# Kernel optimization log

Measured on AMD Instinct MI355X. Metric: run time of the kernel, lower is better.

## Reference

```python
import jax, jax.numpy as jnp
import numpy as np

IN_F = 4096
OUT_F = 4096
Q_RANK = 2
R_RANK = 2
SCALE = 1.0
B, S = 2, 2048


def setup_inputs() -> dict:
    key = jax.random.key(0)
    ks = jax.random.split(key, 8)
    inp = jax.random.normal(ks[0], (B, S, IN_F), jnp.float32)
    # Q, R come from a QR decomposition of linear.weight.t(); random stand-ins with
    # matching shapes and O(1) scale are fine for a numerical baseline.
    Q = jax.random.normal(ks[1], (IN_F, OUT_F), jnp.float32) / np.sqrt(IN_F).astype(np.float32)
    R = jax.random.normal(ks[2], (OUT_F, OUT_F), jnp.float32) / np.sqrt(OUT_F).astype(np.float32)
    # kron_Q1/Q2 are initialized to identity in __init__ (never re-initialized);
    # add small noise so the rotation path is non-trivial.
    sq1 = IN_F // Q_RANK
    kron_Q1 = jnp.eye(sq1, dtype=jnp.float32) + 0.01 * jax.random.normal(ks[3], (sq1, sq1), jnp.float32)
    kron_Q2 = jnp.eye(Q_RANK, dtype=jnp.float32) + 0.01 * jax.random.normal(ks[4], (Q_RANK, Q_RANK), jnp.float32)
    # kron_R1/R2 use normal init with std = 1/size.
    sr1 = OUT_F // R_RANK
    kron_R1 = jax.random.normal(ks[5], (sr1, sr1), jnp.float32) / sr1
    kron_R2 = jax.random.normal(ks[6], (R_RANK, R_RANK), jnp.float32) / R_RANK
    # lambda_matrix inits to zeros; use small noise so the delta term is exercised.
    lambda_matrix = 0.01 * jax.random.normal(ks[7], (OUT_F,), jnp.float32)
    return {"input": inp, "Q": Q, "R": R, "kron_Q1": kron_Q1, "kron_Q2": kron_Q2,
            "kron_R1": kron_R1, "kron_R2": kron_R2, "lambda_matrix": lambda_matrix}


def reference(input, Q, R, kron_Q1, kron_Q2, kron_R1, kron_R2, lambda_matrix):
    rotation = jnp.kron(kron_Q1, kron_Q2)          # [in, in]
    orth = jnp.kron(kron_R1, kron_R2)              # [out, out]
    # orth @ diag(lambda) @ orth.T without materializing diag
    R_eff = R + (orth * lambda_matrix[None, :]) @ orth.T  # [out, out]
    W_t = rotation @ (Q @ R_eff)                   # [in, out]
    # F.linear(input, W_t.t()) == input @ W_t; dropout is identity in eval; bias=False
    return (input @ W_t) * SCALE
```

## Files before the change

kernel.cpp:

```cpp
#include <hip/hip_runtime.h>
#include <stdint.h>


typedef unsigned short u16;
typedef short bf16x8 __attribute__((ext_vector_type(8)));
typedef float f32x4 __attribute__((ext_vector_type(4)));

__device__ __forceinline__ u16 f2bf(float f) {
  union { float f; uint32_t u; } v; v.f = f;
  return (u16)((v.u + 0x7FFFu + ((v.u >> 16) & 1u)) >> 16);
}

__device__ __forceinline__ void store_out(float* p, float v) { *p = v; }
__device__ __forceinline__ void store_out(u16* p, float v) { *p = f2bf(v); }

__device__ __forceinline__ void gload_lds16(const u16* g, u16* l) {
  __builtin_amdgcn_global_load_lds(
      (__attribute__((address_space(1))) void*)(uintptr_t)g,
      (__attribute__((address_space(3))) void*)l, 16, 0, 0);
}

#define MFMA16(a, b, c) __builtin_amdgcn_mfma_f32_16x16x32_bf16((a), (b), (c), 0, 0, 0)

template <typename OutT>
__global__ __launch_bounds__(512, 2) void gemm256(
    const u16* __restrict__ A, const u16* __restrict__ Bt, OutT* __restrict__ C,
    int M, int N, int K, int ldC, long long sA, long long sB, long long sC) {
  extern __shared__ __align__(16) u16 smem[];
  u16* ldsA = smem;
  u16* ldsB = smem + 32768;

  const int tid  = (int)threadIdx.x;
  const int lane = tid & 63;
  const int wid  = tid >> 6;
  const int wr   = wid >> 2;
  const int wc   = wid & 3;

  const int tilesX = (int)gridDim.x;
  const int tilesXY = tilesX * (int)gridDim.y;
  const int nwg = tilesXY * (int)gridDim.z;
  const int bid = ((int)blockIdx.z * (int)gridDim.y + (int)blockIdx.y) * tilesX + (int)blockIdx.x;
  const int swz = (bid & 7) * (nwg >> 3) + (bid >> 3);
  const int z   = swz / tilesXY;
  const int rem = swz % tilesXY;
  const int brow = (rem / tilesX) << 8;
  const int bcol = (rem % tilesX) << 8;
  A += (size_t)z * sA;
  Bt += (size_t)(z >> 1) * sB;
  C += (size_t)z * sC;

  const int lr = lane & 15, lg = lane >> 4, h = lr >> 1;
  const int sf = (lg + ((lr & 1) << 2)) ^ h;
  const int abase = wr * 8192 + h * 64 + sf * 8;
  const int bbase = (wc >> 1) * 8192 + ((wc & 1) * 32 + h) * 64 + sf * 8;

  const int kp   = (tid & 7) ^ ((tid >> 3) & 7);
  const int srow = 2 * (tid >> 3) + (kp >> 2);
  const int scol = (kp & 3) << 3;
  const size_t gA0 = (size_t)(brow + srow) * K + scol;
  const size_t gB0 = (size_t)(bcol + srow) * K + scol;
  const size_t rstep = (size_t)K << 7;
  const int sdst = wid * 512;

  const int NC = K >> 6;
  const int NI = NC >> 1;

  f32x4 acc[8][4] = {};
  bf16x8 af[4], bf[4][2];

#define STG_A(t, rh, ks) gload_lds16(A + gA0 + (rh) * rstep + (size_t)(t) * 64 + (ks) * 32, \
    ldsA + ((t) & 1) * 16384 + (rh) * 8192 + (ks) * 4096 + sdst)
#define STG_B(t, rh, ks) gload_lds16(Bt + gB0 + (rh) * rstep + (size_t)(t) * 64 + (ks) * 32, \
    ldsB + ((t) & 1) * 16384 + (rh) * 8192 + (ks) * 4096 + sdst)
#define VM4 asm volatile("s_waitcnt vmcnt(4)" ::: "memory")
#define VM0 asm volatile("s_waitcnt vmcnt(0)" ::: "memory")

#define PH(BUF, MH, KS, RDBF, S0, S1, TAIL) do {                                \
    const u16* _pa = ldsA + (BUF) * 16384 + abase + (KS) * 4096;                \
    const u16* _pb = ldsB + (BUF) * 16384 + bbase + (KS) * 4096;                \
    _Pragma("unroll")                                                           \
    for (int m = 0; m < 4; ++m)                                                 \
      af[m] = *(const bf16x8*)(_pa + ((MH) * 4 + m) * 512);                     \
    if (RDBF) {                                                                 \
      _Pragma("unroll")                                                         \
      for (int n = 0; n < 4; ++n)                                               \
        bf[n][KS] = *(const bf16x8*)(_pb + n * 512);                            \
    }                                                                           \
    S0; S1;                                                                     \
    __builtin_amdgcn_s_barrier();                                               \
    asm volatile("s_waitcnt lgkmcnt(0)" ::: "memory");                          \
    __builtin_amdgcn_sched_barrier(0);                                          \
    __builtin_amdgcn_s_setprio(1);                                              \
    _Pragma("unroll")                                                           \
    for (int m = 0; m < 4; ++m)                                                 \
      _Pragma("unroll")                                                         \
      for (int n = 0; n < 4; ++n)                                               \
        acc[(MH) * 4 + m][n] = MFMA16(af[m], bf[n][KS], acc[(MH) * 4 + m][n]);  \
    __builtin_amdgcn_s_setprio(0);                                              \
    TAIL;                                                                       \
    __builtin_amdgcn_sched_barrier(0);                                          \
    __builtin_amdgcn_s_barrier();                                               \
  } while (0)

  STG_A(0, 0, 0); STG_A(0, 0, 1); STG_A(0, 1, 0); STG_A(0, 1, 1);
  STG_B(0, 0, 0); STG_B(0, 0, 1); STG_B(0, 1, 0); STG_B(0, 1, 1);
  STG_B(1, 0, 0); STG_B(1, 0, 1); STG_B(1, 1, 0); STG_B(1, 1, 1);
  VM4;
  __builtin_amdgcn_sched_barrier(0);
  __builtin_amdgcn_s_barrier();

  for (int i = 0; i < NI - 1; ++i) {
    const int tn = 2 * i;
    PH(0, 0, 0, 1, STG_A(tn + 1, 0, 0), STG_A(tn + 1, 0, 1), (void)0);
    PH(0, 0, 1, 1, STG_A(tn + 1, 1, 0), STG_A(tn + 1, 1, 1), (void)0);
    PH(0, 1, 0, 0, STG_B(tn + 2, 0, 0), STG_B(tn + 2, 0, 1), (void)0);
    PH(0, 1, 1, 0, STG_B(tn + 2, 1, 0), STG_B(tn + 2, 1, 1), VM4);
    PH(1, 0, 0, 1, STG_A(tn + 2, 0, 0), STG_A(tn + 2, 0, 1), (void)0);
    PH(1, 0, 1, 1, STG_A(tn + 2, 1, 0), STG_A(tn + 2, 1, 1), (void)0);
    PH(1, 1, 0, 0, STG_B(tn + 3, 0, 0), STG_B(tn + 3, 0, 1), (void)0);
    PH(1, 1, 1, 0, STG_B(tn + 3, 1, 0), STG_B(tn + 3, 1, 1), VM4);
  }
  {
    PH(0, 0, 0, 1, STG_A(NC - 1, 0, 0), STG_A(NC - 1, 0, 1), (void)0);
    PH(0, 0, 1, 1, STG_A(NC - 1, 1, 0), STG_A(NC - 1, 1, 1), (void)0);
    PH(0, 1, 0, 0, (void)0, (void)0, (void)0);
    PH(0, 1, 1, 0, (void)0, (void)0, VM0);
    PH(1, 0, 0, 1, (void)0, (void)0, (void)0);
    PH(1, 0, 1, 1, (void)0, (void)0, (void)0);
    PH(1, 1, 0, 0, (void)0, (void)0, (void)0);
    PH(1, 1, 1, 0, (void)0, (void)0, (void)0);
  }

#undef PH
#undef STG_A
#undef STG_B
#undef VM4
#undef VM0

#pragma unroll
  for (int m = 0; m < 8; ++m) {
    const int r0 = brow + wr * 128 + m * 16 + lg * 4;
#pragma unroll
    for (int n = 0; n < 4; ++n) {
      const int cc = bcol + wc * 64 + n * 16 + lr;
#pragma unroll
      for (int j = 0; j < 4; ++j)
        store_out(&C[(size_t)(r0 + j) * ldC + cc], acc[m][n][j]);
    }
  }
}

__global__ void trans_kernel(const float* __restrict__ in, u16* __restrict__ out, int n) {
  __shared__ float t[32][33];
  const int bx = (int)blockIdx.x * 32, by = (int)blockIdx.y * 32;
  const int x = (int)threadIdx.x, y0 = (int)threadIdx.y;
#pragma unroll
  for (int dy = 0; dy < 32; dy += 8)
    t[y0 + dy][x] = in[(size_t)(bx + y0 + dy) * n + by + x];
  __syncthreads();
#pragma unroll
  for (int dy = 0; dy < 32; dy += 8)
    out[(size_t)(by + y0 + dy) * n + bx + x] = f2bf(t[x][y0 + dy]);
}

__global__ void transperm_kernel(const float* __restrict__ in, u16* __restrict__ out) {
  __shared__ float t[32][33];
  const int bx = (int)blockIdx.x * 32, by = (int)blockIdx.y * 32;
  const int x = (int)threadIdx.x, y0 = (int)threadIdx.y;
#pragma unroll
  for (int dy = 0; dy < 32; dy += 8)
    t[y0 + dy][x] = in[(size_t)(bx + y0 + dy) * 4096 + by + x];
  __syncthreads();
  const int r = bx + x;
  const int cp = ((r & 1) << 11) | (r >> 1);
#pragma unroll
  for (int dy = 0; dy < 32; dy += 8)
    out[(size_t)(by + y0 + dy) * 4096 + cp] = f2bf(t[x][y0 + dy]);
}

__global__ void transadd_kernel(const float* __restrict__ R, const float* __restrict__ Dsub,
                                const float* __restrict__ R2, u16* __restrict__ out) {
  __shared__ float t[32][33];
  const int bx = (int)blockIdx.x * 32, by = (int)blockIdx.y * 32;
  const int x = (int)threadIdx.x, y0 = (int)threadIdx.y;
#pragma unroll
  for (int dy = 0; dy < 32; dy += 8)
    t[y0 + dy][x] = R[(size_t)(bx + y0 + dy) * 4096 + by + x];
  __syncthreads();
  const float r20 = R2[0], r21 = R2[1], r22 = R2[2], r23 = R2[3];
  const int j = bx + x;
  const float cj0 = (j & 1) ? r22 : r20;
  const float cj1 = (j & 1) ? r23 : r21;
#pragma unroll
  for (int dy = 0; dy < 32; dy += 8) {
    const int i = by + y0 + dy;
    const float ci0 = (i & 1) ? r22 : r20;
    const float ci1 = (i & 1) ? r23 : r21;
    const size_t o = ((size_t)(i >> 1) << 11) + (j >> 1);
    const float de = Dsub[o] + Dsub[o + 2u * 4194304u];
    const float dd = Dsub[o + 4194304u] + Dsub[o + 3u * 4194304u];
    const float d = ci0 * cj0 * de + ci1 * cj1 * dd;
    out[(size_t)i * 4096 + j] = f2bf(t[x][y0 + dy] + d);
  }
}

__global__ void scale_r1_kernel(const float* __restrict__ R1, const float* __restrict__ lam,
                                u16* __restrict__ B2, u16* __restrict__ A4) {
  const int idx = (int)blockIdx.x * 256 + (int)threadIdx.x;
  const int i1 = idx >> 9, k1 = (idx & 511) << 2;
  const float4 r1 = *(const float4*)(R1 + (size_t)i1 * 2048 + k1);
  const float4 l0 = *(const float4*)(lam + 2 * k1);
  const float4 l1 = *(const float4*)(lam + 2 * k1 + 4);
  const int kh = k1 >> 10, kk = k1 & 1023;
  const size_t off = (size_t)i1 * 1024 + kk;
  const size_t P = 2097152;
  ushort4 rb, eb, ob;
  rb.x = f2bf(r1.x); rb.y = f2bf(r1.y); rb.z = f2bf(r1.z); rb.w = f2bf(r1.w);
  eb.x = f2bf(r1.x * l0.x); eb.y = f2bf(r1.y * l0.z);
  eb.z = f2bf(r1.z * l1.x); eb.w = f2bf(r1.w * l1.z);
  ob.x = f2bf(r1.x * l0.y); ob.y = f2bf(r1.y * l0.w);
  ob.z = f2bf(r1.z * l1.y); ob.w = f2bf(r1.w * l1.w);
  *(ushort4*)(B2 + (size_t)kh * P + off) = rb;
  *(ushort4*)(A4 + (size_t)(kh * 2) * P + off) = eb;
  *(ushort4*)(A4 + (size_t)(kh * 2 + 1) * P + off) = ob;
}

__global__ void tprep_kernel(const float* __restrict__ in, const float* __restrict__ Q2,
                             u16* __restrict__ T) {
  const int idx = (int)blockIdx.x * 256 + (int)threadIdx.x;
  const int s = idx >> 9, k1 = (idx & 511) << 2;
  const float4 a = *(const float4*)(in + (size_t)s * 4096 + 2 * k1);
  const float4 b = *(const float4*)(in + (size_t)s * 4096 + 2 * k1 + 4);
  const float e[4] = {a.x, a.z, b.x, b.z};
  const float o[4] = {a.y, a.w, b.y, b.w};
  const float q00 = Q2[0], q01 = Q2[1], q10 = Q2[2], q11 = Q2[3];
  ushort4 t0, t1;
  t0.x = f2bf(e[0] * q00 + o[0] * q10); t1.x = f2bf(e[0] * q01 + o[0] * q11);
  t0.y = f2bf(e[1] * q00 + o[1] * q10); t1.y = f2bf(e[1] * q01 + o[1] * q11);
  t0.z = f2bf(e[2] * q00 + o[2] * q10); t1.z = f2bf(e[2] * q01 + o[2] * q11);
  t0.w = f2bf(e[3] * q00 + o[3] * q10); t1.w = f2bf(e[3] * q01 + o[3] * q11);
  *(ushort4*)(T + (size_t)s * 2048 + k1) = t0;
  *(ushort4*)(T + 8388608 + (size_t)s * 2048 + k1) = t1;
}

extern "C" void kernel_launch(void* const* d_in, const int* in_sizes, int n_in,
                              void* d_out, int out_size, void* d_ws, size_t ws_size,
                              hipStream_t stream) {
  const float* input = (const float*)d_in[0];
  const float* Q     = (const float*)d_in[1];
  const float* R     = (const float*)d_in[2];
  const float* Q1    = (const float*)d_in[3];
  const float* Q2    = (const float*)d_in[4];
  const float* R1    = (const float*)d_in[5];
  const float* R2    = (const float*)d_in[6];
  const float* lam   = (const float*)d_in[7];
  float* out = (float*)d_out;

  const size_t MB = 1024ull * 1024ull;
  char* ws = (char*)d_ws;
  u16* B2    = (u16*)(ws + 0 * MB);
  u16* A4    = (u16*)(ws + 8 * MB);
  u16* Q1tb  = (u16*)(ws + 24 * MB);
  u16* T     = (u16*)(ws + 32 * MB);
  u16* Qtp   = (u16*)(ws + 64 * MB);
  u16* rteff = (u16*)(ws + 96 * MB);
  u16* X1p   = (u16*)(ws + 128 * MB);
  u16* X2    = (u16*)(ws + 8 * MB);
  float* Dsub = (float*)d_out;

  {
    void (*pf)(const u16*, const u16*, float*, int, int, int, int, long long, long long, long long) = gemm256<float>;
    void (*pb)(const u16*, const u16*, u16*, int, int, int, int, long long, long long, long long)   = gemm256<u16>;
    (void)hipFuncSetAttribute((const void*)pf, hipFuncAttributeMaxDynamicSharedMemorySize, 131072);
    (void)hipFuncSetAttribute((const void*)pb, hipFuncAttributeMaxDynamicSharedMemorySize, 131072);
  }

  const dim3 tb(32, 8);
  trans_kernel<<<dim3(64, 64), tb, 0, stream>>>(Q1, Q1tb, 2048);
  transperm_kernel<<<dim3(128, 128), tb, 0, stream>>>(Q, Qtp);
  scale_r1_kernel<<<4096, 256, 0, stream>>>(R1, lam, B2, A4);
  tprep_kernel<<<8192, 256, 0, stream>>>(input, Q2, T);
  gemm256<float><<<dim3(8, 8, 4), 512, 131072, stream>>>(
      A4, B2, Dsub, 2048, 2048, 1024, 2048, 2097152LL, 2097152LL, 4194304LL);
  transadd_kernel<<<dim3(128, 128), tb, 0, stream>>>(R, Dsub, R2, rteff);
  gemm256<u16><<<dim3(8, 16, 2), 512, 131072, stream>>>(
      T, Q1tb, X1p, 4096, 2048, 2048, 4096, 8388608LL, 0LL, 2048LL);
  gemm256<u16><<<dim3(16, 16, 1), 512, 131072, stream>>>(
      X1p, Qtp, X2, 4096, 4096, 4096, 4096, 0LL, 0LL, 0LL);
  gemm256<float><<<dim3(16, 16, 1), 512, 131072, stream>>>(
      X2, rteff, out, 4096, 4096, 4096, 4096, 0LL, 0LL, 0LL);
}
```

Measured before the change: 431.9 us.

## Shrink GEMM tile to 256x128 with triple-buffered BK=32 LDS pipeline

Reworks the bf16 MFMA GEMM from a 256x256 tile with double-buffered BK=64 stages to a 256x128 tile with a rotating three-buffer BK=32 pipeline. The 8 waves become a 4x2 grid, each computing 64x64, and all launch grids double in N. LDS drops to 72KB and launch bounds rise to 4 blocks per CU, aiming for more occupancy and better wave-level latency hiding. The costs are lower arithmetic intensity per tile, more global and L2 traffic for A, and a barrier pair every 32-wide k step.

Measured after the change: 510.5 us. 1.18x slower.

```diff
diff --git a/kernel.cpp b/kernel.cpp
--- a/kernel.cpp
+++ b/kernel.cpp
@@ -23,18 +23,18 @@
 #define MFMA16(a, b, c) __builtin_amdgcn_mfma_f32_16x16x32_bf16((a), (b), (c), 0, 0, 0)
 
 template <typename OutT>
-__global__ __launch_bounds__(512, 2) void gemm256(
+__global__ __launch_bounds__(512, 4) void gemm256(
     const u16* __restrict__ A, const u16* __restrict__ Bt, OutT* __restrict__ C,
     int M, int N, int K, int ldC, long long sA, long long sB, long long sC) {
   extern __shared__ __align__(16) u16 smem[];
   u16* ldsA = smem;
-  u16* ldsB = smem + 32768;
+  u16* ldsB = smem + 24576;
 
   const int tid  = (int)threadIdx.x;
   const int lane = tid & 63;
   const int wid  = tid >> 6;
-  const int wr   = wid >> 2;
-  const int wc   = wid & 3;
+  const int wr   = wid >> 1;
+  const int wc   = wid & 1;
 
   const int tilesX = (int)gridDim.x;
   const int tilesXY = tilesX * (int)gridDim.y;
@@ -44,15 +44,15 @@
   const int z   = swz / tilesXY;
   const int rem = swz % tilesXY;
   const int brow = (rem / tilesX) << 8;
-  const int bcol = (rem % tilesX) << 8;
+  const int bcol = (rem % tilesX) << 7;
   A += (size_t)z * sA;
   Bt += (size_t)(z >> 1) * sB;
   C += (size_t)z * sC;
 
   const int lr = lane & 15, lg = lane >> 4, h = lr >> 1;
   const int sf = (lg + ((lr & 1) << 2)) ^ h;
-  const int abase = wr * 8192 + h * 64 + sf * 8;
-  const int bbase = (wc >> 1) * 8192 + ((wc & 1) * 32 + h) * 64 + sf * 8;
+  const int abase = (wr >> 1) * 4096 + (wr & 1) * 2048 + h * 64 + sf * 8;
+  const int bbase = wc * 2048 + h * 64 + sf * 8;
 
   const int kp   = (tid & 7) ^ ((tid >> 3) & 7);
   const int srow = 2 * (tid >> 3) + (kp >> 2);
@@ -62,31 +62,35 @@
   const size_t rstep = (size_t)K << 7;
   const int sdst = wid * 512;
 
-  const int NC = K >> 6;
-  const int NI = NC >> 1;
-
-  f32x4 acc[8][4] = {};
-  bf16x8 af[4], bf[4][2];
-
-#define STG_A(t, rh, ks) gload_lds16(A + gA0 + (rh) * rstep + (size_t)(t) * 64 + (ks) * 32, \
-    ldsA + ((t) & 1) * 16384 + (rh) * 8192 + (ks) * 4096 + sdst)
-#define STG_B(t, rh, ks) gload_lds16(Bt + gB0 + (rh) * rstep + (size_t)(t) * 64 + (ks) * 32, \
-    ldsB + ((t) & 1) * 16384 + (rh) * 8192 + (ks) * 4096 + sdst)
-#define VM4 asm volatile("s_waitcnt vmcnt(4)" ::: "memory")
+  const int NC = K >> 5;
+
+  f32x4 acc[4][4] = {};
+  bf16x8 af[4], bf[4];
+
+  int aCur = 0, aNxt = 8192, aSpr = 16384;
+  int bCur = 0, bNxt = 4096, bSpr = 8192;
+
+#define STG_A(c, rh, dstOff) gload_lds16(A + gA0 + (rh) * rstep + (size_t)(c) * 32, \
+    ldsA + (dstOff) + (rh) * 4096 + sdst)
+#define STG_B(c, dstOff) gload_lds16(Bt + gB0 + (size_t)(c) * 32, ldsB + (dstOff) + sdst)
+#define STAGE(c, aOff, bOff) do { STG_A(c, 0, aOff); STG_A(c, 1, aOff); STG_B(c, bOff); } while (0)
+#define VM3 asm volatile("s_waitcnt vmcnt(3)" ::: "memory")
 #define VM0 asm volatile("s_waitcnt vmcnt(0)" ::: "memory")
 
-#define PH(BUF, MH, KS, RDBF, S0, S1, TAIL) do {                                \
-    const u16* _pa = ldsA + (BUF) * 16384 + abase + (KS) * 4096;                \
-    const u16* _pb = ldsB + (BUF) * 16384 + bbase + (KS) * 4096;                \
+  STAGE(0, 0, 0);
+  STAGE(1, 8192, 4096);
+  VM3;
+  __builtin_amdgcn_sched_barrier(0);
+  __builtin_amdgcn_s_barrier();
+
+#define PH(DOSTG, c2, TAIL) do {                                                \
+    const u16* _pa = ldsA + aCur + abase;                                       \
+    const u16* _pb = ldsB + bCur + bbase;                                       \
     _Pragma("unroll")                                                           \
-    for (int m = 0; m < 4; ++m)                                                 \
-      af[m] = *(const bf16x8*)(_pa + ((MH) * 4 + m) * 512);                     \
-    if (RDBF) {                                                                 \
-      _Pragma("unroll")                                                         \
-      for (int n = 0; n < 4; ++n)                                               \
-        bf[n][KS] = *(const bf16x8*)(_pb + n * 512);                            \
-    }                                                                           \
-    S0; S1;                                                                     \
+    for (int m = 0; m < 4; ++m) af[m] = *(const bf16x8*)(_pa + m * 512);        \
+    _Pragma("unroll")                                                           \
+    for (int n = 0; n < 4; ++n) bf[n] = *(const bf16x8*)(_pb + n * 512);        \
+    if (DOSTG) STAGE(c2, aSpr, bSpr);                                           \
     __builtin_amdgcn_s_barrier();                                               \
     asm volatile("s_waitcnt lgkmcnt(0)" ::: "memory");                          \
     __builtin_amdgcn_sched_barrier(0);                                          \
@@ -95,51 +99,29 @@
     for (int m = 0; m < 4; ++m)                                                 \
       _Pragma("unroll")                                                         \
       for (int n = 0; n < 4; ++n)                                               \
-        acc[(MH) * 4 + m][n] = MFMA16(af[m], bf[n][KS], acc[(MH) * 4 + m][n]);  \
+        acc[m][n] = MFMA16(af[m], bf[n], acc[m][n]);                            \
     __builtin_amdgcn_s_setprio(0);                                              \
     TAIL;                                                                       \
     __builtin_amdgcn_sched_barrier(0);                                          \
     __builtin_amdgcn_s_barrier();                                               \
+    const int _ta = aCur; aCur = aNxt; aNxt = aSpr; aSpr = _ta;                 \
+    const int _tb = bCur; bCur = bNxt; bNxt = bSpr; bSpr = _tb;                 \
   } while (0)
 
-  STG_A(0, 0, 0); STG_A(0, 0, 1); STG_A(0, 1, 0); STG_A(0, 1, 1);
-  STG_B(0, 0, 0); STG_B(0, 0, 1); STG_B(0, 1, 0); STG_B(0, 1, 1);
-  STG_B(1, 0, 0); STG_B(1, 0, 1); STG_B(1, 1, 0); STG_B(1, 1, 1);
-  VM4;
-  __builtin_amdgcn_sched_barrier(0);
-  __builtin_amdgcn_s_barrier();
-
-  for (int i = 0; i < NI - 1; ++i) {
-    const int tn = 2 * i;
-    PH(0, 0, 0, 1, STG_A(tn + 1, 0, 0), STG_A(tn + 1, 0, 1), (void)0);
-    PH(0, 0, 1, 1, STG_A(tn + 1, 1, 0), STG_A(tn + 1, 1, 1), (void)0);
-    PH(0, 1, 0, 0, STG_B(tn + 2, 0, 0), STG_B(tn + 2, 0, 1), (void)0);
-    PH(0, 1, 1, 0, STG_B(tn + 2, 1, 0), STG_B(tn + 2, 1, 1), VM4);
-    PH(1, 0, 0, 1, STG_A(tn + 2, 0, 0), STG_A(tn + 2, 0, 1), (void)0);
-    PH(1, 0, 1, 1, STG_A(tn + 2, 1, 0), STG_A(tn + 2, 1, 1), (void)0);
-    PH(1, 1, 0, 0, STG_B(tn + 3, 0, 0), STG_B(tn + 3, 0, 1), (void)0);
-    PH(1, 1, 1, 0, STG_B(tn + 3, 1, 0), STG_B(tn + 3, 1, 1), VM4);
-  }
-  {
-    PH(0, 0, 0, 1, STG_A(NC - 1, 0, 0), STG_A(NC - 1, 0, 1), (void)0);
-    PH(0, 0, 1, 1, STG_A(NC - 1, 1, 0), STG_A(NC - 1, 1, 1), (void)0);
-    PH(0, 1, 0, 0, (void)0, (void)0, (void)0);
-    PH(0, 1, 1, 0, (void)0, (void)0, VM0);
-    PH(1, 0, 0, 1, (void)0, (void)0, (void)0);
-    PH(1, 0, 1, 1, (void)0, (void)0, (void)0);
-    PH(1, 1, 0, 0, (void)0, (void)0, (void)0);
-    PH(1, 1, 1, 0, (void)0, (void)0, (void)0);
-  }
+  for (int c = 0; c < NC - 2; ++c) PH(1, c + 2, VM3);
+  PH(0, 0, VM0);
+  PH(0, 0, (void)0);
 
 #undef PH
+#undef STAGE
 #undef STG_A
 #undef STG_B
-#undef VM4
+#undef VM3
 #undef VM0
 
 #pragma unroll
-  for (int m = 0; m < 8; ++m) {
-    const int r0 = brow + wr * 128 + m * 16 + lg * 4;
+  for (int m = 0; m < 4; ++m) {
+    const int r0 = brow + wr * 64 + m * 16 + lg * 4;
 #pragma unroll
     for (int n = 0; n < 4; ++n) {
       const int cc = bcol + wc * 64 + n * 16 + lr;
@@ -271,8 +253,8 @@
   {
     void (*pf)(const u16*, const u16*, float*, int, int, int, int, long long, long long, long long) = gemm256<float>;
     void (*pb)(const u16*, const u16*, u16*, int, int, int, int, long long, long long, long long)   = gemm256<u16>;
-    (void)hipFuncSetAttribute((const void*)pf, hipFuncAttributeMaxDynamicSharedMemorySize, 131072);
-    (void)hipFuncSetAttribute((const void*)pb, hipFuncAttributeMaxDynamicSharedMemorySize, 131072);
+    (void)hipFuncSetAttribute((const void*)pf, hipFuncAttributeMaxDynamicSharedMemorySize, 73728);
+    (void)hipFuncSetAttribute((const void*)pb, hipFuncAttributeMaxDynamicSharedMemorySize, 73728);
   }
 
   const dim3 tb(32, 8);
@@ -280,13 +262,13 @@
   transperm_kernel<<<dim3(128, 128), tb, 0, stream>>>(Q, Qtp);
   scale_r1_kernel<<<4096, 256, 0, stream>>>(R1, lam, B2, A4);
   tprep_kernel<<<8192, 256, 0, stream>>>(input, Q2, T);
-  gemm256<float><<<dim3(8, 8, 4), 512, 131072, stream>>>(
+  gemm256<float><<<dim3(16, 8, 4), 512, 73728, stream>>>(
       A4, B2, Dsub, 2048, 2048, 1024, 2048, 2097152LL, 2097152LL, 4194304LL);
   transadd_kernel<<<dim3(128, 128), tb, 0, stream>>>(R, Dsub, R2, rteff);
-  gemm256<u16><<<dim3(8, 16, 2), 512, 131072, stream>>>(
+  gemm256<u16><<<dim3(16, 16, 2), 512, 73728, stream>>>(
       T, Q1tb, X1p, 4096, 2048, 2048, 4096, 8388608LL, 0LL, 2048LL);
-  gemm256<u16><<<dim3(16, 16, 1), 512, 131072, stream>>>(
+  gemm256<u16><<<dim3(32, 16, 1), 512, 73728, stream>>>(
       X1p, Qtp, X2, 4096, 4096, 4096, 4096, 0LL, 0LL, 0LL);
-  gemm256<float><<<dim3(16, 16, 1), 512, 131072, stream>>>(
+  gemm256<float><<<dim3(32, 16, 1), 512, 73728, stream>>>(
       X2, rteff, out, 4096, 4096, 4096, 4096, 0LL, 0LL, 0LL);
 }
```
